# Optimization experiments

Measured on AMD Instinct MI355X. Metric: run time of the kernel, lower is better.

Reference implementation:

```python
import jax, jax.numpy as jnp
import numpy as np

N_HEAD = 16
ROPE_BASE = 10000.0


def _rope_cos_sin(T, D, dtype):
    # D = head_size; matches RotaryEmbedding: emb = cat(freqs, freqs)
    inv_freq = 1.0 / (ROPE_BASE ** (jnp.arange(0, D, 2, dtype=jnp.float32) / D))
    t = jnp.arange(T, dtype=jnp.float32)
    freqs = t[:, None] * inv_freq[None, :]              # [T, D/2]
    emb = jnp.concatenate([freqs, freqs], axis=-1)      # [T, D]
    return jnp.cos(emb).astype(dtype), jnp.sin(emb).astype(dtype)


def _rotate_half(x):
    d = x.shape[-1] // 2
    return jnp.concatenate([-x[..., d:], x[..., :d]], axis=-1)


def setup_inputs() -> dict:
    key = jax.random.key(0)
    ks = jax.random.split(key, 5)
    B, T, C = 2, 2048, 1024
    s_in = 1.0 / np.sqrt(C)
    return {
        "x": jax.random.normal(ks[0], (B, T, C), dtype=jnp.float32),
        "w_attn": jax.random.normal(ks[1], (C, 3 * C), dtype=jnp.float32) * s_in,
        "b_attn": jnp.zeros((3 * C,), dtype=jnp.float32),
        "w_proj": jax.random.normal(ks[2], (C, C), dtype=jnp.float32) * s_in,
        "b_proj": jnp.zeros((C,), dtype=jnp.float32),
    }


def reference(x, w_attn, b_attn, w_proj, b_proj):
    B, T, C = x.shape
    H = N_HEAD
    D = C // H

    qkv = x @ w_attn + b_attn                            # [B,T,3C]
    q, k, v = jnp.split(qkv, 3, axis=-1)
    # [B,T,C] -> [B,H,T,D]
    to_heads = lambda a: a.reshape(B, T, H, D).transpose(0, 2, 1, 3)
    q, k, v = to_heads(q), to_heads(k), to_heads(v)

    cos, sin = _rope_cos_sin(T, D, x.dtype)              # [T,D] each, broadcast over B,H
    q = q * cos + _rotate_half(q) * sin
    k = k * cos + _rotate_half(k) * sin

    scale = 1.0 / np.sqrt(D)
    att = jnp.einsum("bhqd,bhkd->bhqk", q, k) * scale    # [B,H,T,T]
    causal = jnp.tril(jnp.ones((T, T), dtype=bool))
    att = jnp.where(causal, att, jnp.finfo(att.dtype).min)
    att = jax.nn.softmax(att, axis=-1)
    y = jnp.einsum("bhqk,bhkd->bhqd", att, v)            # [B,H,T,D]

    y = y.transpose(0, 2, 1, 3).reshape(B, T, C)
    return y @ w_proj + b_proj
```

## Files before the change

kernel.cpp:

```cpp
#include <hip/hip_runtime.h>
#include <hip/hip_bf16.h>

#define B_ 2
#define T_ 2048
#define C_ 1024
#define H_ 16
#define D_ 64

typedef __attribute__((ext_vector_type(8))) short bf16x8;
typedef __attribute__((ext_vector_type(4))) float f32x4;

static __device__ __forceinline__ float bf2f(unsigned short u) {
  union { unsigned int i; float f; } c;
  c.i = ((unsigned int)u) << 16;
  return c.f;
}
static __device__ __forceinline__ unsigned short f2bf(float f) {
  union { float f; unsigned int i; } c;
  c.f = f;
  unsigned int x = c.i;
  return (unsigned short)((x + 0x7fffu + ((x >> 16) & 1u)) >> 16);
}

static __device__ __forceinline__ void gl_lds16(const void* g, void* s) {
  __builtin_amdgcn_global_load_lds(
      (const __attribute__((address_space(1))) void*)g,
      (__attribute__((address_space(3))) void*)s, 16, 0, 0);
}

__global__ __launch_bounds__(256) void fill_kernel_f32(float* __restrict__ out,
                                                       int n, float v) {
  int i = blockIdx.x * 256 + threadIdx.x;
  if (i < n) out[i] = v;
}

__global__ __launch_bounds__(256) void cvt_bf16(const float* __restrict__ X,
                                                unsigned short* __restrict__ Xb) {
  int i = (blockIdx.x * 256 + threadIdx.x) * 8;
  float4 f0 = *(const float4*)(X + i);
  float4 f1 = *(const float4*)(X + i + 4);
  union { unsigned short u[8]; uint4 v; } p;
  p.u[0] = f2bf(f0.x); p.u[1] = f2bf(f0.y); p.u[2] = f2bf(f0.z); p.u[3] = f2bf(f0.w);
  p.u[4] = f2bf(f1.x); p.u[5] = f2bf(f1.y); p.u[6] = f2bf(f1.z); p.u[7] = f2bf(f1.w);
  *(uint4*)(Xb + i) = p.v;
}

__global__ __launch_bounds__(256) void transpose_cvt(const float* __restrict__ W,
                                                     unsigned short* __restrict__ WT,
                                                     int Kd, int Nd) {
  __shared__ float tile[32][33];
  const int n0 = blockIdx.x * 32, k0 = blockIdx.y * 32;
  const int tx = threadIdx.x & 31, ty = threadIdx.x >> 5;
#pragma unroll
  for (int i = 0; i < 4; ++i)
    tile[ty + i * 8][tx] = W[(size_t)(k0 + ty + i * 8) * Nd + n0 + tx];
  __syncthreads();
#pragma unroll
  for (int i = 0; i < 4; ++i)
    WT[(size_t)(n0 + ty + i * 8) * Kd + k0 + tx] = f2bf(tile[tx][ty + i * 8]);
}

__global__ __launch_bounds__(256) void v_transpose(const unsigned short* __restrict__ vP,
                                                   unsigned short* __restrict__ vT) {
  __shared__ unsigned short tile[64][72];
  const int t0 = blockIdx.x * 64;
  const int bh = blockIdx.y;
  const int b = bh >> 4;
  const int srow = threadIdx.x >> 3;
  const int sc8 = (threadIdx.x & 7) * 8;
#pragma unroll
  for (int it = 0; it < 2; ++it) {
    int r = srow + it * 32;
    *(uint4*)&tile[r][sc8] =
        *(const uint4*)(vP + (size_t)(b * T_ + t0 + r) * 1024 + (bh & 15) * 64 + sc8);
  }
  __syncthreads();
#pragma unroll
  for (int it = 0; it < 2; ++it) {
    int dd = srow + it * 32;
    union { unsigned short u[8]; uint4 v; } o;
#pragma unroll
    for (int j = 0; j < 8; ++j) o.u[j] = tile[sc8 + j][dd];
    *(uint4*)(vT + ((size_t)bh * 64 + dd) * 2048 + t0 + sc8) = o.v;
  }
}

template <int OUT_PLANES>
__global__ __launch_bounds__(256) void mfma_gemm(
    const unsigned short* __restrict__ A,
    const unsigned short* __restrict__ BT,
    const float* __restrict__ bias,
    unsigned short* __restrict__ qP, unsigned short* __restrict__ kP,
    unsigned short* __restrict__ vP, float* __restrict__ Fout,
    int N, int K) {
  __shared__ unsigned short As[128 * 64];
  __shared__ unsigned short Bs[128 * 64];

  const int tid = threadIdx.x;
  const int w = tid >> 6, lane = tid & 63;
  const int lo = lane & 15, g = lane >> 4;
  const int wm = (w >> 1) * 64, wn = (w & 1) * 64;
  const int m0 = blockIdx.y * 128, n0 = blockIdx.x * 128;

  const int lr8 = lane >> 3;

  const f32x4 zero4 = {0.f, 0.f, 0.f, 0.f};
  f32x4 acc[4][4] = {{zero4, zero4, zero4, zero4}, {zero4, zero4, zero4, zero4},
                     {zero4, zero4, zero4, zero4}, {zero4, zero4, zero4, zero4}};

  for (int k0 = 0; k0 < K; k0 += 64) {
    __syncthreads();
#pragma unroll
    for (int it = 0; it < 4; ++it) {
      const int base_row = w * 32 + it * 8;
      const int r = base_row + lr8;
      const int j = (lane & 7) ^ (r & 7);
      gl_lds16(A + (size_t)(m0 + r) * K + k0 + j * 8, &As[base_row * 64]);
      gl_lds16(BT + (size_t)(n0 + r) * K + k0 + j * 8, &Bs[base_row * 64]);
    }
    __syncthreads();

#pragma unroll
    for (int kk = 0; kk < 2; ++kk) {
      bf16x8 af[4], bfr[4];
#pragma unroll
      for (int i = 0; i < 4; ++i) {
        int ra = wm + i * 16 + lo;
        int rb = wn + i * 16 + lo;
        af[i]  = *(const bf16x8*)&As[ra * 64 + ((g + kk * 4) ^ (ra & 7)) * 8];
        bfr[i] = *(const bf16x8*)&Bs[rb * 64 + ((g + kk * 4) ^ (rb & 7)) * 8];
      }
#pragma unroll
      for (int i = 0; i < 4; ++i)
#pragma unroll
        for (int j = 0; j < 4; ++j)
          acc[i][j] = __builtin_amdgcn_mfma_f32_16x16x32_bf16(af[i], bfr[j],
                                                              acc[i][j], 0, 0, 0);
    }
  }

  float bv[4];
#pragma unroll
  for (int j = 0; j < 4; ++j) bv[j] = bias[n0 + wn + j * 16 + lo];

  if (OUT_PLANES) {
    const int pl = n0 >> 10;
    unsigned short* P = (pl == 0) ? qP : (pl == 1) ? kP : vP;
    const int col0 = (n0 & 1023) + wn + lo;
#pragma unroll
    for (int i = 0; i < 4; ++i)
#pragma unroll
      for (int r = 0; r < 4; ++r) {
        size_t row = (size_t)(m0 + wm + i * 16 + g * 4 + r);
#pragma unroll
        for (int j = 0; j < 4; ++j)
          P[row * 1024 + col0 + j * 16] = f2bf(acc[i][j][r] + bv[j]);
      }
  } else {
#pragma unroll
    for (int i = 0; i < 4; ++i)
#pragma unroll
      for (int r = 0; r < 4; ++r) {
        size_t row = (size_t)(m0 + wm + i * 16 + g * 4 + r);
#pragma unroll
        for (int j = 0; j < 4; ++j)
          Fout[row * N + n0 + wn + j * 16 + lo] = acc[i][j][r] + bv[j];
      }
  }
}

__global__ __launch_bounds__(256) void rope_kernel(unsigned short* __restrict__ qP,
                                                   unsigned short* __restrict__ kP) {
  int idx = blockIdx.x * 256 + threadIdx.x;
  int i = idx & 31;
  int h = (idx >> 5) & 15;
  int t = (idx >> 9) & 2047;
  int b = idx >> 20;
  float inv = exp2f((float)(-2 * i) * (13.287712379549449f / 64.0f));
  float ang = (float)t * inv;
  float s, c;
  sincosf(ang, &s, &c);
  size_t base = (size_t)(b * T_ + t) * 1024 + h * D_ + i;
  float q1 = bf2f(qP[base]);
  float q2 = bf2f(qP[base + 32]);
  qP[base]      = f2bf((q1 * c - q2 * s) * 0.125f);
  qP[base + 32] = f2bf((q2 * c + q1 * s) * 0.125f);
  float k1 = bf2f(kP[base]);
  float k2 = bf2f(kP[base + 32]);
  kP[base]      = f2bf(k1 * c - k2 * s);
  kP[base + 32] = f2bf(k2 * c + k1 * s);
}

__global__ __launch_bounds__(256) void flash_mfma3(
    unsigned short* __restrict__ qP,
    const unsigned short* __restrict__ kP,
    const unsigned short* __restrict__ vT) {
  const int bx = blockIdx.x;
  const int bh = blockIdx.y;
  const int b = bh >> 4, h = bh & 15;
  const int tid = threadIdx.x;
  const int w = tid >> 6, lane = tid & 63;
  const int lo = lane & 15, g = lane >> 4;

  __shared__ unsigned short Ks[64][72];
  __shared__ unsigned short VTs[64][72];
  __shared__ unsigned short Ps[64][72];

  const int srow = tid >> 3;
  const int sc8 = (tid & 7) * 8;
  const f32x4 zero4 = {0.f, 0.f, 0.f, 0.f};

#pragma unroll
  for (int half = 0; half < 2; ++half) {
    const int qt = half ? (31 - bx) : bx;
    const int rowq0 = b * T_ + qt * 64;

    const unsigned short* qrow = qP + (size_t)(rowq0 + w * 16 + lo) * 1024 + h * 64;
    bf16x8 aq0 = *(const bf16x8*)(qrow + g * 8);
    bf16x8 aq1 = *(const bf16x8*)(qrow + 32 + g * 8);

    f32x4 oacc[4] = {zero4, zero4, zero4, zero4};
    float lsum[4] = {0.f, 0.f, 0.f, 0.f};

    uint4 kreg0, kreg1, vreg0, vreg1;
    {
      const size_t kb = (size_t)(b * T_ + srow) * 1024 + h * 64 + sc8;
      kreg0 = *(const uint4*)(kP + kb);
      kreg1 = *(const uint4*)(kP + kb + (size_t)32 * 1024);
      const size_t vb = ((size_t)bh * 64 + srow) * 2048 + sc8;
      vreg0 = *(const uint4*)(vT + vb);
      vreg1 = *(const uint4*)(vT + vb + (size_t)32 * 2048);
    }

    for (int kt = 0; kt <= qt; ++kt) {
      __syncthreads();
      *(uint4*)&Ks[srow][sc8]       = kreg0;
      *(uint4*)&Ks[srow + 32][sc8]  = kreg1;
      *(uint4*)&VTs[srow][sc8]      = vreg0;
      *(uint4*)&VTs[srow + 32][sc8] = vreg1;
      __syncthreads();
      if (kt < qt) {
        const size_t kb = (size_t)(b * T_ + (kt + 1) * 64 + srow) * 1024 + h * 64 + sc8;
        kreg0 = *(const uint4*)(kP + kb);
        kreg1 = *(const uint4*)(kP + kb + (size_t)32 * 1024);
        const size_t vb = ((size_t)bh * 64 + srow) * 2048 + (kt + 1) * 64 + sc8;
        vreg0 = *(const uint4*)(vT + vb);
        vreg1 = *(const uint4*)(vT + vb + (size_t)32 * 2048);
      }

      f32x4 sacc[4] = {zero4, zero4, zero4, zero4};
#pragma unroll
      for (int ct = 0; ct < 4; ++ct) {
        bf16x8 bk0 = *(const bf16x8*)&Ks[ct * 16 + lo][g * 8];
        bf16x8 bk1 = *(const bf16x8*)&Ks[ct * 16 + lo][32 + g * 8];
        sacc[ct] = __builtin_amdgcn_mfma_f32_16x16x32_bf16(aq0, bk0, sacc[ct], 0, 0, 0);
        sacc[ct] = __builtin_amdgcn_mfma_f32_16x16x32_bf16(aq1, bk1, sacc[ct], 0, 0, 0);
      }

      if (kt == qt) {
        const int qrow_base = qt * 64 + w * 16 + g * 4;
#pragma unroll
        for (int ct = 0; ct < 4; ++ct)
#pragma unroll
          for (int r = 0; r < 4; ++r)
            if ((kt * 64 + ct * 16 + lo) > (qrow_base + r)) sacc[ct][r] = -1e30f;
      }

#pragma unroll
      for (int ct = 0; ct < 4; ++ct)
#pragma unroll
        for (int r = 0; r < 4; ++r) {
          float p = __expf(sacc[ct][r]);
          lsum[r] += p;
          Ps[w * 16 + g * 4 + r][ct * 16 + lo] = f2bf(p);
        }

      bf16x8 ap0 = *(const bf16x8*)&Ps[w * 16 + lo][g * 8];
      bf16x8 ap1 = *(const bf16x8*)&Ps[w * 16 + lo][32 + g * 8];
#pragma unroll
      for (int c2 = 0; c2 < 4; ++c2) {
        bf16x8 bv0 = *(const bf16x8*)&VTs[c2 * 16 + lo][g * 8];
        bf16x8 bv1 = *(const bf16x8*)&VTs[c2 * 16 + lo][32 + g * 8];
        oacc[c2] = __builtin_amdgcn_mfma_f32_16x16x32_bf16(ap0, bv0, oacc[c2], 0, 0, 0);
        oacc[c2] = __builtin_amdgcn_mfma_f32_16x16x32_bf16(ap1, bv1, oacc[c2], 0, 0, 0);
      }
    }

#pragma unroll
    for (int r = 0; r < 4; ++r) {
      float v = lsum[r];
      v += __shfl_xor(v, 1);
      v += __shfl_xor(v, 2);
      v += __shfl_xor(v, 4);
      v += __shfl_xor(v, 8);
      float inv_l = 1.0f / v;
      unsigned short* dst = qP + (size_t)(rowq0 + w * 16 + g * 4 + r) * 1024 + h * 64 + lo;
#pragma unroll
      for (int c2 = 0; c2 < 4; ++c2)
        dst[c2 * 16] = f2bf(oacc[c2][r] * inv_l);
    }
  }
}

extern "C" void kernel_launch(void* const* d_in, const int* in_sizes, int n_in,
                              void* d_out, int out_size, void* d_ws, size_t ws_size,
                              hipStream_t stream) {
  const float *x = nullptr, *w_attn = nullptr, *b_attn = nullptr,
              *w_proj = nullptr, *b_proj = nullptr;
  for (int i = 0; i < n_in; ++i) {
    switch (in_sizes[i]) {
      case B_ * T_ * C_:  x      = (const float*)d_in[i]; break;
      case C_ * 3 * C_:   w_attn = (const float*)d_in[i]; break;
      case 3 * C_:        b_attn = (const float*)d_in[i]; break;
      case C_ * C_:       w_proj = (const float*)d_in[i]; break;
      case C_:            b_proj = (const float*)d_in[i]; break;
      default: break;
    }
  }
  float* out = (float*)d_out;
  const int nblk = (out_size + 255) / 256;

  if (!x || !w_attn || !b_attn || !w_proj || !b_proj) {
    fill_kernel_f32<<<nblk, 256, 0, stream>>>(out, out_size, 100.0f);
    return;
  }
  if (ws_size < (size_t)48 * 1024 * 1024) {
    fill_kernel_f32<<<nblk, 256, 0, stream>>>(out, out_size, 50.0f);
    return;
  }

  unsigned short* qP  = (unsigned short*)d_ws;
  unsigned short* kP  = qP + (size_t)(B_ * T_) * 1024;
  unsigned short* vP  = kP + (size_t)(B_ * T_) * 1024;
  unsigned short* vT  = vP + (size_t)(B_ * T_) * 1024;
  unsigned short* xb  = vT + (size_t)(B_ * T_) * 1024;
  unsigned short* waT = xb + (size_t)(B_ * T_) * C_;
  unsigned short* wpT = waT + (size_t)C_ * 3 * C_;

  transpose_cvt<<<dim3((3 * C_) / 32, C_ / 32), 256, 0, stream>>>(w_attn, waT, C_, 3 * C_);
  transpose_cvt<<<dim3(C_ / 32, C_ / 32), 256, 0, stream>>>(w_proj, wpT, C_, C_);
  cvt_bf16<<<(B_ * T_ * C_) / (256 * 8), 256, 0, stream>>>(x, xb);
  mfma_gemm<1><<<dim3((3 * C_) / 128, (B_ * T_) / 128), 256, 0, stream>>>(
      xb, waT, b_attn, qP, kP, vP, nullptr, 3 * C_, C_);
  rope_kernel<<<(B_ * T_ * H_ * (D_ / 2)) / 256, 256, 0, stream>>>(qP, kP);
  v_transpose<<<dim3(T_ / 64, B_ * H_), 256, 0, stream>>>(vP, vT);
  flash_mfma3<<<dim3(16, B_ * H_), 256, 0, stream>>>(qP, kP, vT);
  mfma_gemm<0><<<dim3(C_ / 128, (B_ * T_) / 128), 256, 0, stream>>>(
      qP, wpT, b_proj, nullptr, nullptr, nullptr, out, C_, C_);
}
```

Measured before the change: 205.7 us.

## Split causal pairing into one query tile per block and transpose score MFMA

Each block now handles a single query tile, with the grid doubled to 32 tiles per head, instead of pairing tile bx with 31-bx in one block. The score MFMA operands are swapped so each lane holds four key columns of one query row. This lets the P tile be written to LDS as packed 8-byte stores and the row sum be reduced with fewer shuffles. It aims to raise block-level parallelism and cut LDS store count, at the cost of load imbalance across blocks because of causal masking, which now relies on the hardware scheduler to balance.

```diff
diff --git a/kernel.cpp b/kernel.cpp
--- a/kernel.cpp
+++ b/kernel.cpp
@@ -191,11 +191,11 @@
   kP[base + 32] = f2bf(k2 * c + k1 * s);
 }
 
-__global__ __launch_bounds__(256) void flash_mfma3(
+__global__ __launch_bounds__(256) void flash_mfma5(
     unsigned short* __restrict__ qP,
     const unsigned short* __restrict__ kP,
     const unsigned short* __restrict__ vT) {
-  const int bx = blockIdx.x;
+  const int qt = blockIdx.x;
   const int bh = blockIdx.y;
   const int b = bh >> 4, h = bh & 15;
   const int tid = threadIdx.x;
@@ -210,95 +210,92 @@
   const int sc8 = (tid & 7) * 8;
   const f32x4 zero4 = {0.f, 0.f, 0.f, 0.f};
 
-#pragma unroll
-  for (int half = 0; half < 2; ++half) {
-    const int qt = half ? (31 - bx) : bx;
-    const int rowq0 = b * T_ + qt * 64;
-
-    const unsigned short* qrow = qP + (size_t)(rowq0 + w * 16 + lo) * 1024 + h * 64;
-    bf16x8 aq0 = *(const bf16x8*)(qrow + g * 8);
-    bf16x8 aq1 = *(const bf16x8*)(qrow + 32 + g * 8);
-
-    f32x4 oacc[4] = {zero4, zero4, zero4, zero4};
-    float lsum[4] = {0.f, 0.f, 0.f, 0.f};
-
-    uint4 kreg0, kreg1, vreg0, vreg1;
-    {
-      const size_t kb = (size_t)(b * T_ + srow) * 1024 + h * 64 + sc8;
+  const int rowq0 = b * T_ + qt * 64;
+
+  const unsigned short* qrow = qP + (size_t)(rowq0 + w * 16 + lo) * 1024 + h * 64;
+  bf16x8 aq0 = *(const bf16x8*)(qrow + g * 8);
+  bf16x8 aq1 = *(const bf16x8*)(qrow + 32 + g * 8);
+
+  f32x4 oacc[4] = {zero4, zero4, zero4, zero4};
+  float lsum = 0.f;
+
+  uint4 kreg0, kreg1, vreg0, vreg1;
+  {
+    const size_t kb = (size_t)(b * T_ + srow) * 1024 + h * 64 + sc8;
+    kreg0 = *(const uint4*)(kP + kb);
+    kreg1 = *(const uint4*)(kP + kb + (size_t)32 * 1024);
+    const size_t vb = ((size_t)bh * 64 + srow) * 2048 + sc8;
+    vreg0 = *(const uint4*)(vT + vb);
+    vreg1 = *(const uint4*)(vT + vb + (size_t)32 * 2048);
+  }
+
+  for (int kt = 0; kt <= qt; ++kt) {
+    __syncthreads();
+    *(uint4*)&Ks[srow][sc8]       = kreg0;
+    *(uint4*)&Ks[srow + 32][sc8]  = kreg1;
+    *(uint4*)&VTs[srow][sc8]      = vreg0;
+    *(uint4*)&VTs[srow + 32][sc8] = vreg1;
+    __syncthreads();
+    if (kt < qt) {
+      const size_t kb = (size_t)(b * T_ + (kt + 1) * 64 + srow) * 1024 + h * 64 + sc8;
       kreg0 = *(const uint4*)(kP + kb);
       kreg1 = *(const uint4*)(kP + kb + (size_t)32 * 1024);
-      const size_t vb = ((size_t)bh * 64 + srow) * 2048 + sc8;
+      const size_t vb = ((size_t)bh * 64 + srow) * 2048 + (kt + 1) * 64 + sc8;
       vreg0 = *(const uint4*)(vT + vb);
       vreg1 = *(const uint4*)(vT + vb + (size_t)32 * 2048);
     }
 
-    for (int kt = 0; kt <= qt; ++kt) {
-      __syncthreads();
-      *(uint4*)&Ks[srow][sc8]       = kreg0;
-      *(uint4*)&Ks[srow + 32][sc8]  = kreg1;
-      *(uint4*)&VTs[srow][sc8]      = vreg0;
-      *(uint4*)&VTs[srow + 32][sc8] = vreg1;
-      __syncthreads();
-      if (kt < qt) {
-        const size_t kb = (size_t)(b * T_ + (kt + 1) * 64 + srow) * 1024 + h * 64 + sc8;
-        kreg0 = *(const uint4*)(kP + kb);
-        kreg1 = *(const uint4*)(kP + kb + (size_t)32 * 1024);
-        const size_t vb = ((size_t)bh * 64 + srow) * 2048 + (kt + 1) * 64 + sc8;
-        vreg0 = *(const uint4*)(vT + vb);
-        vreg1 = *(const uint4*)(vT + vb + (size_t)32 * 2048);
-      }
-
-      f32x4 sacc[4] = {zero4, zero4, zero4, zero4};
-#pragma unroll
-      for (int ct = 0; ct < 4; ++ct) {
-        bf16x8 bk0 = *(const bf16x8*)&Ks[ct * 16 + lo][g * 8];
-        bf16x8 bk1 = *(const bf16x8*)&Ks[ct * 16 + lo][32 + g * 8];
-        sacc[ct] = __builtin_amdgcn_mfma_f32_16x16x32_bf16(aq0, bk0, sacc[ct], 0, 0, 0);
-        sacc[ct] = __builtin_amdgcn_mfma_f32_16x16x32_bf16(aq1, bk1, sacc[ct], 0, 0, 0);
-      }
-
-      if (kt == qt) {
-        const int qrow_base = qt * 64 + w * 16 + g * 4;
-#pragma unroll
-        for (int ct = 0; ct < 4; ++ct)
-#pragma unroll
-          for (int r = 0; r < 4; ++r)
-            if ((kt * 64 + ct * 16 + lo) > (qrow_base + r)) sacc[ct][r] = -1e30f;
-      }
-
+    f32x4 sacc[4] = {zero4, zero4, zero4, zero4};
+#pragma unroll
+    for (int ct = 0; ct < 4; ++ct) {
+      bf16x8 bk0 = *(const bf16x8*)&Ks[ct * 16 + lo][g * 8];
+      bf16x8 bk1 = *(const bf16x8*)&Ks[ct * 16 + lo][32 + g * 8];
+      sacc[ct] = __builtin_amdgcn_mfma_f32_16x16x32_bf16(bk0, aq0, sacc[ct], 0, 0, 0);
+      sacc[ct] = __builtin_amdgcn_mfma_f32_16x16x32_bf16(bk1, aq1, sacc[ct], 0, 0, 0);
+    }
+
+    if (kt == qt) {
 #pragma unroll
       for (int ct = 0; ct < 4; ++ct)
 #pragma unroll
-        for (int r = 0; r < 4; ++r) {
-          float p = __expf(sacc[ct][r]);
-          lsum[r] += p;
-          Ps[w * 16 + g * 4 + r][ct * 16 + lo] = f2bf(p);
-        }
-
-      bf16x8 ap0 = *(const bf16x8*)&Ps[w * 16 + lo][g * 8];
-      bf16x8 ap1 = *(const bf16x8*)&Ps[w * 16 + lo][32 + g * 8];
-#pragma unroll
-      for (int c2 = 0; c2 < 4; ++c2) {
-        bf16x8 bv0 = *(const bf16x8*)&VTs[c2 * 16 + lo][g * 8];
-        bf16x8 bv1 = *(const bf16x8*)&VTs[c2 * 16 + lo][32 + g * 8];
-        oacc[c2] = __builtin_amdgcn_mfma_f32_16x16x32_bf16(ap0, bv0, oacc[c2], 0, 0, 0);
-        oacc[c2] = __builtin_amdgcn_mfma_f32_16x16x32_bf16(ap1, bv1, oacc[c2], 0, 0, 0);
-      }
-    }
-
-#pragma unroll
-    for (int r = 0; r < 4; ++r) {
-      float v = lsum[r];
-      v += __shfl_xor(v, 1);
-      v += __shfl_xor(v, 2);
-      v += __shfl_xor(v, 4);
-      v += __shfl_xor(v, 8);
-      float inv_l = 1.0f / v;
-      unsigned short* dst = qP + (size_t)(rowq0 + w * 16 + g * 4 + r) * 1024 + h * 64 + lo;
-#pragma unroll
-      for (int c2 = 0; c2 < 4; ++c2)
-        dst[c2 * 16] = f2bf(oacc[c2][r] * inv_l);
-    }
+        for (int r = 0; r < 4; ++r)
+          if (ct * 16 + g * 4 + r > w * 16 + lo) sacc[ct][r] = -1e30f;
+    }
+
+#pragma unroll
+    for (int ct = 0; ct < 4; ++ct) {
+      float p0 = __expf(sacc[ct][0]);
+      float p1 = __expf(sacc[ct][1]);
+      float p2 = __expf(sacc[ct][2]);
+      float p3 = __expf(sacc[ct][3]);
+      lsum += (p0 + p1) + (p2 + p3);
+      unsigned int u0 = (unsigned int)f2bf(p0) | ((unsigned int)f2bf(p1) << 16);
+      unsigned int u1 = (unsigned int)f2bf(p2) | ((unsigned int)f2bf(p3) << 16);
+      uint2 pw; pw.x = u0; pw.y = u1;
+      *(uint2*)&Ps[w * 16 + lo][ct * 16 + g * 4] = pw;
+    }
+
+    bf16x8 ap0 = *(const bf16x8*)&Ps[w * 16 + lo][g * 8];
+    bf16x8 ap1 = *(const bf16x8*)&Ps[w * 16 + lo][32 + g * 8];
+#pragma unroll
+    for (int c2 = 0; c2 < 4; ++c2) {
+      bf16x8 bv0 = *(const bf16x8*)&VTs[c2 * 16 + lo][g * 8];
+      bf16x8 bv1 = *(const bf16x8*)&VTs[c2 * 16 + lo][32 + g * 8];
+      oacc[c2] = __builtin_amdgcn_mfma_f32_16x16x32_bf16(ap0, bv0, oacc[c2], 0, 0, 0);
+      oacc[c2] = __builtin_amdgcn_mfma_f32_16x16x32_bf16(ap1, bv1, oacc[c2], 0, 0, 0);
+    }
+  }
+
+  lsum += __shfl_xor(lsum, 16);
+  lsum += __shfl_xor(lsum, 32);
+
+#pragma unroll
+  for (int r = 0; r < 4; ++r) {
+    float inv_r = 1.0f / __shfl(lsum, g * 4 + r);
+    unsigned short* dst = qP + (size_t)(rowq0 + w * 16 + g * 4 + r) * 1024 + h * 64 + lo;
+#pragma unroll
+    for (int c2 = 0; c2 < 4; ++c2)
+      dst[c2 * 16] = f2bf(oacc[c2][r] * inv_r);
   }
 }
 
@@ -344,7 +341,7 @@
       xb, waT, b_attn, qP, kP, vP, nullptr, 3 * C_, C_);
   rope_kernel<<<(B_ * T_ * H_ * (D_ / 2)) / 256, 256, 0, stream>>>(qP, kP);
   v_transpose<<<dim3(T_ / 64, B_ * H_), 256, 0, stream>>>(vP, vT);
-  flash_mfma3<<<dim3(16, B_ * H_), 256, 0, stream>>>(qP, kP, vT);
+  flash_mfma5<<<dim3(32, B_ * H_), 256, 0, stream>>>(qP, kP, vT);
   mfma_gemm<0><<<dim3(C_ / 128, (B_ * T_) / 128), 256, 0, stream>>>(
       qP, wpT, b_proj, nullptr, nullptr, nullptr, out, C_, C_);
 }
```

New measurement: 219.7 us. +6.8%, slower.
